# Kernel optimization log

Hardware: AMD Instinct MI355X
Metric: run time of the kernel (lower is better)

The kernel has to match this reference:

```python
import jax, jax.numpy as jnp
import numpy as np

N = 100000   # nodes of ntype 'gene'
E = 800000   # edges per metapath
D = 256      # input_dim == output_dim
H = 4        # attn heads
C = D // H   # out_channels per head
M = 2        # num metapaths (tail relations = M + 1, last = self)


def _lrelu(x):
    return jnp.where(x >= 0, x, 0.2 * x)


def _segment_softmax(logits, seg, num_segments):
    # logits: [E, H], seg: [E] int targets
    mx = jax.ops.segment_max(logits, seg, num_segments=num_segments)
    mx = jnp.where(jnp.isfinite(mx), mx, 0.0)  # empty segments -> 0
    ex = jnp.exp(logits - mx[seg])
    den = jax.ops.segment_sum(ex, seg, num_segments=num_segments)
    return ex / (den[seg] + 1e-16)


def setup_inputs() -> dict:
    key = jax.random.key(0)
    ks = jax.random.split(key, 10)
    s = 1.0 / np.sqrt(D)
    return {
        "x": jax.random.normal(ks[0], (N, D), dtype=jnp.float32),
        "edge_index0": jax.random.randint(ks[1], (2, E), 0, N, dtype=jnp.int32),
        "edge_index1": jax.random.randint(ks[2], (2, E), 0, N, dtype=jnp.int32),
        "W_l": jax.random.normal(ks[3], (D, D), dtype=jnp.float32) * s,
        "b_l": jnp.zeros((D,), dtype=jnp.float32),
        "W_r": jax.random.normal(ks[4], (D, D), dtype=jnp.float32) * s,
        "b_r": jnp.zeros((D,), dtype=jnp.float32),
        "attn": jax.random.normal(ks[5], (M, H, 2 * C), dtype=jnp.float32) * (1.0 / np.sqrt(2 * C)),
        "rel_attn_l": jax.random.normal(ks[6], (H, C), dtype=jnp.float32) * (1.0 / np.sqrt(C)),
        "rel_attn_r": jax.random.normal(ks[7], (H, C), dtype=jnp.float32) * (1.0 / np.sqrt(C)),
    }


def reference(x, edge_index0, edge_index1, W_l, b_l, W_r, b_r, attn, rel_attn_l, rel_attn_r):
    # projections -> [N, H, C]  (eval mode: dropout/batchnorm off)
    l = (x @ W_l.T + b_l).reshape(N, H, C)
    r = (x @ W_r.T + b_r).reshape(N, H, C)

    # attn split: first C for x_i (target, r-proj), last C for x_j (source, l-proj);
    # leaky_relu is elementwise so the concat+dot separates exactly.
    def agg(edge_index, m_idx):
        src, tgt = edge_index[0], edge_index[1]
        a_i = jnp.einsum('ehc,hc->eh', _lrelu(r[tgt]), attn[m_idx, :, :C])
        a_j = jnp.einsum('ehc,hc->eh', _lrelu(l[src]), attn[m_idx, :, C:])
        alpha = _segment_softmax(a_i + a_j, tgt, N)          # [E, H]
        msg = l[src] * alpha[:, :, None]                      # [E, H, C]
        return jax.ops.segment_sum(msg, tgt, num_segments=N)  # [N, H, C]

    out0 = agg(edge_index0, 0)
    out1 = agg(edge_index1, 1)
    emb = jnp.stack([out0, out1, r], axis=1)                  # [N, M+1, H, C]

    # relation-level beta attention (get_beta_weights)
    alpha_l = jnp.einsum('nhc,hc->nh', r, rel_attn_l)         # [N, H]
    alpha_r = jnp.einsum('nrhc,hc->nrh', emb, rel_attn_r)     # [N, M+1, H]
    beta = jax.nn.softmax(_lrelu(alpha_l[:, None, :] + alpha_r), axis=1)

    h = (emb * beta[..., None]).sum(axis=1).reshape(N, D)
    return jax.nn.relu(h)
```

## Files before the change

kernel.cpp:

```cpp
#include <hip/hip_runtime.h>
#include <hip/hip_bf16.h>
#include <math.h>

#define D_ 256
#define H_ 4
#define C_ 64

typedef __attribute__((ext_vector_type(8))) short short8;
typedef __attribute__((ext_vector_type(4))) float f32x4;

__device__ inline float lrelu(float v) { return v >= 0.f ? v : 0.2f * v; }

__device__ inline unsigned short f2b(float f) {
    unsigned u = __float_as_uint(f);
    u = (u + 0x7FFFu + ((u >> 16) & 1u)) >> 16;
    return (unsigned short)u;
}
__device__ inline float b2f(unsigned short u) {
    return __uint_as_float(((unsigned)u) << 16);
}

#define GLDS(src, dst) __builtin_amdgcn_global_load_lds(                      \
    (const __attribute__((address_space(1))) void*)(src),                     \
    (__attribute__((address_space(3))) void*)(dst), 16, 0, 0)

__global__ __launch_bounds__(256) void convert_w(
    const float* __restrict__ Wl, const float* __restrict__ Wr,
    unsigned short* __restrict__ Wb)
{
    int i4 = blockIdx.x * 256 + threadIdx.x;
    float4 v = (i4 < 16384) ? ((const float4*)Wl)[i4]
                            : ((const float4*)Wr)[i4 - 16384];
    ushort4 u;
    u.x = f2b(v.x); u.y = f2b(v.y); u.z = f2b(v.z); u.w = f2b(v.w);
    ((ushort4*)Wb)[i4] = u;
}

__device__ __forceinline__ void stage_a(const float* __restrict__ x, float* dst,
                                        int bm, int k0, int wv, int lane, int Mrows)
{
#pragma unroll
    for (int p = 0; p < 4; p++) {
        int ci = (p * 4 + wv) * 64 + lane;
        int row = ci >> 3, cc = ci & 7;
        int gr = bm + row; if (gr >= Mrows) gr = Mrows - 1;
        const float* src = x + (size_t)gr * 256 + k0 + ((cc ^ (row & 7)) << 2);
        GLDS(src, (char*)dst + (size_t)(p * 4 + wv) * 1024);
    }
}
__device__ __forceinline__ void stage_b(const unsigned short* __restrict__ W,
                                        unsigned short* dst, int bn, int k0,
                                        int wv, int lane)
{
#pragma unroll
    for (int p = 0; p < 2; p++) {
        int ci = (p * 4 + wv) * 64 + lane;
        int col = ci >> 2, cc = ci & 3;
        const unsigned short* src = W + (size_t)(bn + col) * 256 + k0 +
                                    ((cc ^ (col & 3)) << 3);
        GLDS(src, (char*)dst + (size_t)(p * 4 + wv) * 1024);
    }
}

template <bool RB16>
__global__ __launch_bounds__(256) void gemm_fused(
    const float* __restrict__ x, const unsigned short* __restrict__ Wb,
    const float* __restrict__ b_l, const float* __restrict__ b_r,
    const float* __restrict__ attn, const float* __restrict__ rel_l,
    const float* __restrict__ rel_r,
    unsigned short* __restrict__ lout, void* __restrict__ rout,
    float2* __restrict__ ej2, float* __restrict__ al, float* __restrict__ rd,
    int Mrows, int nblk)
{
    int hw = blockIdx.x;
    int orig = hw;
    if ((nblk & 7) == 0) {
        int cpx = nblk >> 3;
        orig = (hw & 7) * cpx + (hw >> 3);
    }
    const int sel = (orig & 3) >> 1;
    const int bn = (orig & 1) * 128;
    const int bm = (orig >> 2) * 128;

    __shared__ float As[2][128 * 32];
    __shared__ unsigned short Bs[2][128 * 32];
    const int tid = threadIdx.x;
    const int lane = tid & 63, wv = tid >> 6;
    const int wr = wv >> 1, wc = wv & 1;
    const unsigned short* W = Wb + (size_t)sel * 65536;

    f32x4 acc[4][4];
#pragma unroll
    for (int m = 0; m < 4; m++)
#pragma unroll
        for (int n = 0; n < 4; n++) acc[m][n] = (f32x4)0.f;

    stage_a(x, As[0], bm, 0, wv, lane, Mrows);
    stage_b(W, Bs[0], bn, 0, wv, lane);
    __syncthreads();

    int cur = 0;
#pragma unroll
    for (int t = 0; t < 8; t++) {
        if (t < 7) {
            stage_a(x, As[cur ^ 1], bm, (t + 1) * 32, wv, lane, Mrows);
            stage_b(W, Bs[cur ^ 1], bn, (t + 1) * 32, wv, lane);
        }
        short8 bfr[4];
#pragma unroll
        for (int n = 0; n < 4; n++) {
            int col = wc * 64 + n * 16 + (lane & 15);
            int sc = (lane >> 4) ^ (col & 3);
            bfr[n] = *(const short8*)&Bs[cur][col * 32 + sc * 8];
        }
        short8 afr[4];
#pragma unroll
        for (int m = 0; m < 4; m++) {
            int row = wr * 64 + m * 16 + (lane & 15);
            int c0 = (lane >> 4) * 2;
            const float* ap = &As[cur][row * 32];
            float4 f0 = *(const float4*)&ap[(c0 ^ (row & 7)) << 2];
            float4 f1 = *(const float4*)&ap[((c0 + 1) ^ (row & 7)) << 2];
            union { short8 v; __hip_bfloat162 b2[4]; } u;
            u.b2[0] = __float22bfloat162_rn(make_float2(f0.x, f0.y));
            u.b2[1] = __float22bfloat162_rn(make_float2(f0.z, f0.w));
            u.b2[2] = __float22bfloat162_rn(make_float2(f1.x, f1.y));
            u.b2[3] = __float22bfloat162_rn(make_float2(f1.z, f1.w));
            afr[m] = u.v;
        }
#pragma unroll
        for (int m = 0; m < 4; m++)
#pragma unroll
            for (int n = 0; n < 4; n++)
                acc[m][n] = __builtin_amdgcn_mfma_f32_16x16x32_bf16(
                    afr[m], bfr[n], acc[m][n], 0, 0, 0);
        __syncthreads();
        cur ^= 1;
    }

    const float* bias = sel ? b_r : b_l;
    const int NH = Mrows * H_;
    const int h = (bn >> 6) + wc;
    float bv[4], w0[4], w1[4], w2[4];
    int gcol[4];
#pragma unroll
    for (int n = 0; n < 4; n++) {
        int c = n * 16 + (lane & 15);
        gcol[n] = bn + wc * 64 + c - (wc * 64 + c) + wc * 64 + c;
        gcol[n] = bn + wc * 64 + c;
        bv[n] = bias[gcol[n]];
        if (sel == 0) {
            w0[n] = attn[(0 * H_ + h) * 128 + 64 + c];
            w1[n] = attn[(1 * H_ + h) * 128 + 64 + c];
            w2[n] = rel_r[h * C_ + c];
        } else {
            w0[n] = rel_l[h * C_ + c];
            w1[n] = rel_r[h * C_ + c];
        }
    }
#pragma unroll
    for (int m = 0; m < 4; m++) {
#pragma unroll
        for (int q = 0; q < 4; q++) {
            int grow = bm + wr * 64 + m * 16 + (lane >> 4) * 4 + q;
            bool ok = grow < Mrows;
            float p0 = 0.f, p1 = 0.f, p2 = 0.f;
#pragma unroll
            for (int n = 0; n < 4; n++) {
                float v = acc[m][n][q] + bv[n];
                if (ok) {
                    if (sel == 0) {
                        lout[(size_t)grow * 256 + gcol[n]] = f2b(v);
                    } else {
                        if (RB16) ((unsigned short*)rout)[(size_t)grow * 256 + gcol[n]] = f2b(v);
                        else      ((float*)rout)[(size_t)grow * 256 + gcol[n]] = v;
                    }
                }
                if (sel == 0) {
                    float lr = lrelu(v);
                    p0 = fmaf(lr, w0[n], p0);
                    p1 = fmaf(lr, w1[n], p1);
                    p2 = fmaf(v, w2[n], p2);
                } else {
                    p0 = fmaf(v, w0[n], p0);
                    p1 = fmaf(v, w1[n], p1);
                }
            }
#pragma unroll
            for (int off = 1; off < 16; off <<= 1) {
                p0 += __shfl_xor(p0, off);
                p1 += __shfl_xor(p1, off);
                if (sel == 0) p2 += __shfl_xor(p2, off);
            }
            if (ok && (lane & 15) == 0) {
                int nh = grow * H_ + h;
                if (sel == 0) {
                    float e0 = __expf(p0), e1 = __expf(p1);
                    ej2[nh]      = make_float2(e0, e0 * p2);
                    ej2[NH + nh] = make_float2(e1, e1 * p2);
                } else {
                    al[nh] = p0;
                    rd[nh] = p1;
                }
            }
        }
    }
}

__global__ __launch_bounds__(256) void edge_hist(
    const int* __restrict__ ei0, const int* __restrict__ ei1,
    int* __restrict__ hist, int E_, int Nn)
{
    int e = blockIdx.x * 256 + threadIdx.x;
    if (e >= E_) return;
    atomicAdd(&hist[ei0[E_ + e]], 1);
    atomicAdd(&hist[Nn + ei1[E_ + e]], 1);
}

__global__ __launch_bounds__(256) void scan_a(
    const int* __restrict__ hist, int* __restrict__ segoff,
    int* __restrict__ bsum, int Nn)
{
    int m = blockIdx.y;
    int gid = blockIdx.x * 256 + threadIdx.x;
    int lane = threadIdx.x & 63, wid = threadIdx.x >> 6;
    int v = (gid < Nn) ? hist[m * Nn + gid] : 0;
    int incl = v;
#pragma unroll
    for (int off = 1; off < 64; off <<= 1) {
        int u = __shfl_up(incl, off);
        if (lane >= off) incl += u;
    }
    __shared__ int ws[4], wo[4];
    if (lane == 63) ws[wid] = incl;
    __syncthreads();
    if (threadIdx.x == 0) {
        int run = 0;
#pragma unroll
        for (int i = 0; i < 4; i++) { wo[i] = run; run += ws[i]; }
        bsum[m * 512 + blockIdx.x] = run;
    }
    __syncthreads();
    if (gid < Nn) segoff[m * Nn + gid] = incl - v + wo[wid];
}

__global__ __launch_bounds__(512) void scan_b(int* __restrict__ bsum, int nb)
{
    int m = blockIdx.x;
    int* b = bsum + m * 512;
    int tid = threadIdx.x, lane = tid & 63, wid = tid >> 6;
    int v = (tid < nb) ? b[tid] : 0;
    int incl = v;
#pragma unroll
    for (int off = 1; off < 64; off <<= 1) {
        int u = __shfl_up(incl, off);
        if (lane >= off) incl += u;
    }
    __shared__ int ws[8], wo[8];
    if (lane == 63) ws[wid] = incl;
    __syncthreads();
    if (tid == 0) {
        int run = 0;
#pragma unroll
        for (int i = 0; i < 8; i++) { wo[i] = run; run += ws[i]; }
    }
    __syncthreads();
    if (tid < nb) b[tid] = incl - v + wo[wid];
}

__global__ __launch_bounds__(256) void edge_scatter(
    const int* __restrict__ ei0, const int* __restrict__ ei1,
    const int* __restrict__ segoff, const int* __restrict__ bsum,
    int* __restrict__ cursor, int* __restrict__ srcs, int E_, int Nn)
{
    int e = blockIdx.x * 256 + threadIdx.x;
    if (e >= E_) return;
    int t0 = ei0[E_ + e];
    int p0 = segoff[t0] + bsum[t0 >> 8] + atomicAdd(&cursor[t0], 1);
    srcs[p0] = ei0[e];
    int t1 = ei1[E_ + e];
    int p1 = segoff[Nn + t1] + bsum[512 + (t1 >> 8)] + atomicAdd(&cursor[Nn + t1], 1);
    srcs[E_ + p1] = ei1[e];
}

template <bool RB16>
__global__ __launch_bounds__(256) void aggregate(
    const int* __restrict__ hist, const int* __restrict__ segoff,
    const int* __restrict__ bsum,
    const int* __restrict__ srcs, const float2* __restrict__ ej2,
    const float* __restrict__ al, const float* __restrict__ rd,
    const void* __restrict__ rv, const unsigned short* __restrict__ l,
    float* __restrict__ out, int Nn, int E_)
{
    __shared__ float4 accS[2][64];
    __shared__ float2 dpS[2][64];
    int lane = threadIdx.x & 63;
    int wid = threadIdx.x >> 6;
    int pair = wid >> 1, mp = wid & 1;
    int t = blockIdx.x * 2 + pair;
    bool active = t < Nn;
    int h = lane >> 4;
    int NH = Nn * H_;
    int nh = t * H_ + h;

    float4 rrow = make_float4(0.f, 0.f, 0.f, 0.f);
    float a = 0.f, rdv = 0.f;
    if (active && mp == 0) {
        if (RB16) {
            ushort4 ru = ((const ushort4*)rv)[(size_t)t * 64 + lane];
            rrow = make_float4(b2f(ru.x), b2f(ru.y), b2f(ru.z), b2f(ru.w));
        } else {
            rrow = ((const float4*)rv)[(size_t)t * 64 + lane];
        }
        a = al[nh];
        rdv = rd[nh];
    }

    float4 acc = make_float4(0.f, 0.f, 0.f, 0.f);
    float den = 0.f, pn = 0.f;
    if (active) {
        int beg = segoff[mp * Nn + t] + bsum[mp * 512 + (t >> 8)];
        int deg = hist[mp * Nn + t];
        const int* sp = srcs + (size_t)mp * E_;
        const float2* ep = ej2 + (size_t)mp * NH;
#pragma unroll 4
        for (int j = 0; j < deg; j++) {
            int s = sp[beg + j];
            float2 v = ep[(size_t)s * H_ + h];
            den += v.x; pn += v.y;
            ushort4 lv = *(const ushort4*)&l[(size_t)s * D_ + lane * 4];
            acc.x = fmaf(b2f(lv.x), v.x, acc.x);
            acc.y = fmaf(b2f(lv.y), v.x, acc.y);
            acc.z = fmaf(b2f(lv.z), v.x, acc.z);
            acc.w = fmaf(b2f(lv.w), v.x, acc.w);
        }
    }
    if (mp == 1) {
        accS[pair][lane] = acc;
        dpS[pair][lane] = make_float2(den, pn);
    }
    __syncthreads();
    if (mp == 1 || !active) return;

    float4 acc1 = accS[pair][lane];
    float2 dp1 = dpS[pair][lane];

    float b0 = lrelu(a + pn / (den + 1e-16f));
    float b1 = lrelu(a + dp1.y / (dp1.x + 1e-16f));
    float b2 = lrelu(a + rdv);
    float mm = fmaxf(b0, fmaxf(b1, b2));
    float e0 = __expf(b0 - mm), e1 = __expf(b1 - mm), e2 = __expf(b2 - mm);
    float inv = 1.f / (e0 + e1 + e2);
    float wm0 = e0 * inv / (den + 1e-16f);
    float wm1 = e1 * inv / (dp1.x + 1e-16f);
    float b2v = e2 * inv;

    float4 o;
    o.x = fmaxf(fmaf(wm0, acc.x, fmaf(wm1, acc1.x, b2v * rrow.x)), 0.f);
    o.y = fmaxf(fmaf(wm0, acc.y, fmaf(wm1, acc1.y, b2v * rrow.y)), 0.f);
    o.z = fmaxf(fmaf(wm0, acc.z, fmaf(wm1, acc1.z, b2v * rrow.z)), 0.f);
    o.w = fmaxf(fmaf(wm0, acc.w, fmaf(wm1, acc1.w, b2v * rrow.w)), 0.f);
    *(float4*)&out[(size_t)t * D_ + lane * 4] = o;
}

extern "C" void kernel_launch(void* const* d_in, const int* in_sizes, int n_in,
                              void* d_out, int out_size, void* d_ws, size_t ws_size,
                              hipStream_t stream) {
    const float* x     = (const float*)d_in[0];
    const int*   ei0   = (const int*)d_in[1];
    const int*   ei1   = (const int*)d_in[2];
    const float* W_l   = (const float*)d_in[3];
    const float* b_l   = (const float*)d_in[4];
    const float* W_r   = (const float*)d_in[5];
    const float* b_r   = (const float*)d_in[6];
    const float* attn  = (const float*)d_in[7];
    const float* rel_l = (const float*)d_in[8];
    const float* rel_r = (const float*)d_in[9];
    float* out = (float*)d_out;

    const int Nn = in_sizes[0] / D_;
    const int E_ = in_sizes[1] / 2;
    const size_t ND = (size_t)Nn * D_;
    const int NH = Nn * H_;

    char* base = (char*)d_ws;
    unsigned short* l = (unsigned short*)base;      size_t off = ND * 2;
    float2* ej2  = (float2*)(base + off); off += (size_t)2 * NH * 8;
    float* al    = (float*)(base + off);  off += (size_t)NH * 4;
    float* rd    = (float*)(base + off);  off += (size_t)NH * 4;
    int* hist    = (int*)(base + off);    off += (size_t)2 * Nn * 4;
    int* cursor  = (int*)(base + off);    off += (size_t)2 * Nn * 4;
    int* segoff  = (int*)(base + off);    off += (size_t)2 * Nn * 4;
    int* bsum    = (int*)(base + off);    off += (size_t)1024 * 4;
    int* srcs    = (int*)(base + off);    off += (size_t)2 * E_ * 4;
    unsigned short* Wb = (unsigned short*)(base + off); off += (size_t)2 * 65536 * 2;
    unsigned short* rb = (unsigned short*)(base + off);
    const bool rb16 = (ws_size >= off + ND * 2);
    void* r_any = rb16 ? (void*)rb : (void*)out;

    hipMemsetAsync(hist, 0, (size_t)4 * Nn * 4, stream);

    convert_w<<<128, 256, 0, stream>>>(W_l, W_r, Wb);

    int rowTiles = (Nn + 127) / 128;
    int nblk = 4 * rowTiles;
    if (rb16)
        gemm_fused<true ><<<nblk, 256, 0, stream>>>(
            x, Wb, b_l, b_r, attn, rel_l, rel_r, l, r_any, ej2, al, rd, Nn, nblk);
    else
        gemm_fused<false><<<nblk, 256, 0, stream>>>(
            x, Wb, b_l, b_r, attn, rel_l, rel_r, l, r_any, ej2, al, rd, Nn, nblk);

    int eb = (E_ + 255) / 256;
    int nb = (Nn + 255) / 256;
    edge_hist<<<eb, 256, 0, stream>>>(ei0, ei1, hist, E_, Nn);
    scan_a<<<dim3(nb, 2), 256, 0, stream>>>(hist, segoff, bsum, Nn);
    scan_b<<<2, 512, 0, stream>>>(bsum, nb);
    edge_scatter<<<eb, 256, 0, stream>>>(ei0, ei1, segoff, bsum, cursor, srcs, E_, Nn);

    if (rb16)
        aggregate<true ><<<(Nn + 1) / 2, 256, 0, stream>>>(
            hist, segoff, bsum, srcs, ej2, al, rd, r_any, l, out, Nn, E_);
    else
        aggregate<false><<<(Nn + 1) / 2, 256, 0, stream>>>(
            hist, segoff, bsum, srcs, ej2, al, rd, r_any, l, out, Nn, E_);
}
```

Baseline: 441.2 us.

## Process both metapaths per wave in aggregate, dropping LDS exchange and barrier

The aggregate kernel now assigns one wave per target node and has that wave loop over both metapaths itself. Previously two waves split the metapaths and combined their results through shared memory and a __syncthreads. The edge loop is also unrolled by two with independent accumulators, so more gathers are in flight per wave. The trade-off is half as many waves working on each node, which gives longer serial chains per wave but removes the barrier and the LDS traffic.

```diff
diff --git a/kernel.cpp b/kernel.cpp
--- a/kernel.cpp
+++ b/kernel.cpp
@@ -146,7 +146,6 @@
 #pragma unroll
     for (int n = 0; n < 4; n++) {
         int c = n * 16 + (lane & 15);
-        gcol[n] = bn + wc * 64 + c - (wc * 64 + c) + wc * 64 + c;
         gcol[n] = bn + wc * 64 + c;
         bv[n] = bias[gcol[n]];
         if (sel == 0) {
@@ -292,74 +291,85 @@
     const void* __restrict__ rv, const unsigned short* __restrict__ l,
     float* __restrict__ out, int Nn, int E_)
 {
-    __shared__ float4 accS[2][64];
-    __shared__ float2 dpS[2][64];
     int lane = threadIdx.x & 63;
-    int wid = threadIdx.x >> 6;
-    int pair = wid >> 1, mp = wid & 1;
-    int t = blockIdx.x * 2 + pair;
-    bool active = t < Nn;
+    int t = blockIdx.x * 4 + (threadIdx.x >> 6);
+    if (t >= Nn) return;
     int h = lane >> 4;
     int NH = Nn * H_;
     int nh = t * H_ + h;
 
-    float4 rrow = make_float4(0.f, 0.f, 0.f, 0.f);
-    float a = 0.f, rdv = 0.f;
-    if (active && mp == 0) {
-        if (RB16) {
-            ushort4 ru = ((const ushort4*)rv)[(size_t)t * 64 + lane];
-            rrow = make_float4(b2f(ru.x), b2f(ru.y), b2f(ru.z), b2f(ru.w));
-        } else {
-            rrow = ((const float4*)rv)[(size_t)t * 64 + lane];
-        }
-        a = al[nh];
-        rdv = rd[nh];
-    }
-
-    float4 acc = make_float4(0.f, 0.f, 0.f, 0.f);
-    float den = 0.f, pn = 0.f;
-    if (active) {
-        int beg = segoff[mp * Nn + t] + bsum[mp * 512 + (t >> 8)];
-        int deg = hist[mp * Nn + t];
-        const int* sp = srcs + (size_t)mp * E_;
-        const float2* ep = ej2 + (size_t)mp * NH;
-#pragma unroll 4
-        for (int j = 0; j < deg; j++) {
-            int s = sp[beg + j];
-            float2 v = ep[(size_t)s * H_ + h];
-            den += v.x; pn += v.y;
-            ushort4 lv = *(const ushort4*)&l[(size_t)s * D_ + lane * 4];
-            acc.x = fmaf(b2f(lv.x), v.x, acc.x);
-            acc.y = fmaf(b2f(lv.y), v.x, acc.y);
-            acc.z = fmaf(b2f(lv.z), v.x, acc.z);
-            acc.w = fmaf(b2f(lv.w), v.x, acc.w);
-        }
-    }
-    if (mp == 1) {
-        accS[pair][lane] = acc;
-        dpS[pair][lane] = make_float2(den, pn);
-    }
-    __syncthreads();
-    if (mp == 1 || !active) return;
-
-    float4 acc1 = accS[pair][lane];
-    float2 dp1 = dpS[pair][lane];
-
-    float b0 = lrelu(a + pn / (den + 1e-16f));
-    float b1 = lrelu(a + dp1.y / (dp1.x + 1e-16f));
+    float4 rrow;
+    if (RB16) {
+        ushort4 ru = ((const ushort4*)rv)[(size_t)t * 64 + lane];
+        rrow = make_float4(b2f(ru.x), b2f(ru.y), b2f(ru.z), b2f(ru.w));
+    } else {
+        rrow = ((const float4*)rv)[(size_t)t * 64 + lane];
+    }
+    float a = al[nh];
+    float rdv = rd[nh];
+
+    float4 accm[2];
+    float denm[2], pnm[2];
+#pragma unroll
+    for (int m = 0; m < 2; m++) {
+        const int* sp = srcs + (size_t)m * E_;
+        const float2* ep = ej2 + (size_t)m * NH;
+        int beg = segoff[m * Nn + t] + bsum[m * 512 + (t >> 8)];
+        int deg = hist[m * Nn + t];
+
+        float4 aA = make_float4(0.f, 0.f, 0.f, 0.f);
+        float4 aB = make_float4(0.f, 0.f, 0.f, 0.f);
+        float dA = 0.f, dB = 0.f, pA = 0.f, pB = 0.f;
+        int j = 0;
+#pragma unroll 2
+        for (; j + 1 < deg; j += 2) {
+            int s0 = sp[beg + j];
+            int s1 = sp[beg + j + 1];
+            float2 v0 = ep[(size_t)s0 * H_ + h];
+            float2 v1 = ep[(size_t)s1 * H_ + h];
+            ushort4 l0 = *(const ushort4*)&l[(size_t)s0 * D_ + lane * 4];
+            ushort4 l1 = *(const ushort4*)&l[(size_t)s1 * D_ + lane * 4];
+            dA += v0.x; pA += v0.y;
+            dB += v1.x; pB += v1.y;
+            aA.x = fmaf(b2f(l0.x), v0.x, aA.x);
+            aA.y = fmaf(b2f(l0.y), v0.x, aA.y);
+            aA.z = fmaf(b2f(l0.z), v0.x, aA.z);
+            aA.w = fmaf(b2f(l0.w), v0.x, aA.w);
+            aB.x = fmaf(b2f(l1.x), v1.x, aB.x);
+            aB.y = fmaf(b2f(l1.y), v1.x, aB.y);
+            aB.z = fmaf(b2f(l1.z), v1.x, aB.z);
+            aB.w = fmaf(b2f(l1.w), v1.x, aB.w);
+        }
+        if (j < deg) {
+            int s0 = sp[beg + j];
+            float2 v0 = ep[(size_t)s0 * H_ + h];
+            ushort4 l0 = *(const ushort4*)&l[(size_t)s0 * D_ + lane * 4];
+            dA += v0.x; pA += v0.y;
+            aA.x = fmaf(b2f(l0.x), v0.x, aA.x);
+            aA.y = fmaf(b2f(l0.y), v0.x, aA.y);
+            aA.z = fmaf(b2f(l0.z), v0.x, aA.z);
+            aA.w = fmaf(b2f(l0.w), v0.x, aA.w);
+        }
+        accm[m] = make_float4(aA.x + aB.x, aA.y + aB.y, aA.z + aB.z, aA.w + aB.w);
+        denm[m] = dA + dB;
+        pnm[m] = pA + pB;
+    }
+
+    float b0 = lrelu(a + pnm[0] / (denm[0] + 1e-16f));
+    float b1 = lrelu(a + pnm[1] / (denm[1] + 1e-16f));
     float b2 = lrelu(a + rdv);
     float mm = fmaxf(b0, fmaxf(b1, b2));
     float e0 = __expf(b0 - mm), e1 = __expf(b1 - mm), e2 = __expf(b2 - mm);
     float inv = 1.f / (e0 + e1 + e2);
-    float wm0 = e0 * inv / (den + 1e-16f);
-    float wm1 = e1 * inv / (dp1.x + 1e-16f);
+    float wm0 = e0 * inv / (denm[0] + 1e-16f);
+    float wm1 = e1 * inv / (denm[1] + 1e-16f);
     float b2v = e2 * inv;
 
     float4 o;
-    o.x = fmaxf(fmaf(wm0, acc.x, fmaf(wm1, acc1.x, b2v * rrow.x)), 0.f);
-    o.y = fmaxf(fmaf(wm0, acc.y, fmaf(wm1, acc1.y, b2v * rrow.y)), 0.f);
-    o.z = fmaxf(fmaf(wm0, acc.z, fmaf(wm1, acc1.z, b2v * rrow.z)), 0.f);
-    o.w = fmaxf(fmaf(wm0, acc.w, fmaf(wm1, acc1.w, b2v * rrow.w)), 0.f);
+    o.x = fmaxf(fmaf(wm0, accm[0].x, fmaf(wm1, accm[1].x, b2v * rrow.x)), 0.f);
+    o.y = fmaxf(fmaf(wm0, accm[0].y, fmaf(wm1, accm[1].y, b2v * rrow.y)), 0.f);
+    o.z = fmaxf(fmaf(wm0, accm[0].z, fmaf(wm1, accm[1].z, b2v * rrow.z)), 0.f);
+    o.w = fmaxf(fmaf(wm0, accm[0].w, fmaf(wm1, accm[1].w, b2v * rrow.w)), 0.f);
     *(float4*)&out[(size_t)t * D_ + lane * 4] = o;
 }
 
@@ -419,9 +429,9 @@
     edge_scatter<<<eb, 256, 0, stream>>>(ei0, ei1, segoff, bsum, cursor, srcs, E_, Nn);
 
     if (rb16)
-        aggregate<true ><<<(Nn + 1) / 2, 256, 0, stream>>>(
+        aggregate<true ><<<(Nn + 3) / 4, 256, 0, stream>>>(
             hist, segoff, bsum, srcs, ej2, al, rd, r_any, l, out, Nn, E_);
     else
-        aggregate<false><<<(Nn + 1) / 2, 256, 0, stream>>>(
+        aggregate<false><<<(Nn + 3) / 4, 256, 0, stream>>>(
             hist, segoff, bsum, srcs, ej2, al, rd, r_any, l, out, Nn, E_);
 }
```

Result: no change. 438.2 us (-0.7%).
